# Performance work log

Measured on AMD Instinct MI355X. Metric: run time of the kernel, lower is better.

The kernel has to match this reference:

```python
import jax, jax.numpy as jnp
import numpy as np

N, K, D, E, H, O = 8192, 16, 256, 128, 512, 256


def _mlp(v, W1, W2):
    # nn.Sequential(Linear(no bias), Tanh, Linear(no bias)) with torch [out,in] weights
    return jnp.tanh(v @ W1.T) @ W2.T


def setup_inputs() -> dict:
    key = jax.random.key(0)
    ks = jax.random.split(key, 16)
    def rn(k, shape, s=1.0):
        return jax.random.normal(k, shape, jnp.float32) * s
    return {
        "x": rn(ks[0], (N, D)),
        "neibs": rn(ks[1], (N * K, D)),
        "edge_emb": rn(ks[2], (N * K, E)),
        "mask": jax.random.randint(ks[3], (N, K), 0, 2, jnp.int32),
        "W1x": rn(ks[4], (H, D), 0.02), "W2x": rn(ks[5], (H, H), 0.02),
        "W1n": rn(ks[6], (H, D), 0.02), "W2n": rn(ks[7], (H, H), 0.02),
        "W1e": rn(ks[8], (H, E), 0.02), "W2e": rn(ks[9], (H, H), 0.02),
        "Wfx": rn(ks[10], (O, D), 0.02), "bfx": jnp.zeros((O,), jnp.float32),
        "Wfn": rn(ks[11], (O, D), 0.02), "bfn": jnp.zeros((O,), jnp.float32),
        "Wfe": rn(ks[12], (O, E), 0.02), "bfe": jnp.zeros((O,), jnp.float32),
    }


def reference(x, neibs, edge_emb, mask, W1x, W2x, W1n, W2n, W1e, W2e,
              Wfx, bfx, Wfn, bfn, Wfe, bfe):
    n, d = x.shape
    e = edge_emb.shape[1]
    x_att = _mlp(x, W1x, W2x)                                  # [N,H]
    neib_att = _mlp(neibs, W1n, W2n).reshape(n, -1, H)         # [N,K,H]
    edge_att = _mlp(edge_emb, W1e, W2e).reshape(n, -1, H)      # [N,K,H]

    # node-neighbor attention (scaled by hard-coded sqrt(512))
    ws = jnp.einsum('nkh,nh->nk', neib_att, x_att) / np.sqrt(512.0).astype(np.float32)
    ws = jax.nn.softmax(ws, axis=1)
    agg_neib = jnp.einsum('nk,nkd->nd', ws, neibs.reshape(n, -1, d))
    out = jnp.concatenate([x @ Wfx.T + bfx, agg_neib @ Wfn.T + bfn], axis=1)

    # node-edge attention (unscaled, masked)
    ws2 = jnp.einsum('nkh,nh->nk', edge_att, x_att)
    ws2 = ws2 + (-9999999.0) * mask.astype(x.dtype)
    ws2 = jax.nn.softmax(ws2, axis=1)
    agg_edge = jnp.einsum('nk,nke->ne', ws2, edge_emb.reshape(n, -1, e))
    out = jnp.concatenate([out, agg_edge @ Wfe.T + bfe], axis=1)  # [N,3*O]
    return jax.nn.relu(out)
```

## Files before the change

### kernel.cpp

```cpp
#include <hip/hip_runtime.h>
#include <hip/hip_bf16.h>

typedef __bf16 bf16;
typedef __bf16 bf16x8 __attribute__((ext_vector_type(8)));
typedef float  f32x4  __attribute__((ext_vector_type(4)));

__device__ __forceinline__ void async16(const bf16* g, bf16* l) {
  __builtin_amdgcn_global_load_lds(
      (__attribute__((address_space(1))) void*)g,
      (__attribute__((address_space(3))) void*)l,
      16, 0, 0);
}

__device__ __forceinline__ void fence_barrier() {
  asm volatile("s_waitcnt vmcnt(0) lgkmcnt(0)" ::: "memory");
  __syncthreads();
}

__device__ __forceinline__ float fast_tanh(float x) {
  float e = __builtin_amdgcn_exp2f(x * 2.88539008177793f);
  return 1.f - 2.f * __builtin_amdgcn_rcpf(e + 1.f);
}

template<int ACT, typename OT>
__global__ __launch_bounds__(256, 4)
void gemm64(const bf16* __restrict__ A, const bf16* __restrict__ W,
            OT* __restrict__ C, int K, int ldc, float alpha,
            const float* __restrict__ bias) {
  __shared__ bf16 As[64 * 64];
  __shared__ bf16 Bs[64 * 64];
  const int tid  = threadIdx.x;
  const int wave = tid >> 6, lane = tid & 63;
  const int wr = wave >> 1, wc = wave & 1;
  const int g = lane >> 4, l4 = lane & 15;

  f32x4 acc[2][2];
#pragma unroll
  for (int i = 0; i < 2; ++i)
#pragma unroll
    for (int j = 0; j < 2; ++j)
      acc[i][j] = (f32x4){0.f, 0.f, 0.f, 0.f};

  const bf16* Abase = A + (size_t)blockIdx.x * 64 * K;
  const bf16* Wbase = W + (size_t)blockIdx.y * 64 * K;

  for (int k0 = 0; k0 < K; k0 += 64) {
#pragma unroll
    for (int i = 0; i < 2; ++i) {
      const int cb  = i * 256 + wave * 64;
      const int c   = cb + lane;
      const int row = c >> 3;
      const int kk  = (c & 7) << 3;
      async16(Abase + (size_t)row * K + k0 + kk, &As[cb * 8]);
      async16(Wbase + (size_t)row * K + k0 + kk, &Bs[cb * 8]);
    }
    fence_barrier();
#pragma unroll
    for (int s = 0; s < 2; ++s) {
      const int koff = s * 32 + g * 8;
      bf16x8 af[2], bfr[2];
#pragma unroll
      for (int i = 0; i < 2; ++i)
        af[i] = *(const bf16x8*)&As[(wr * 32 + i * 16 + l4) * 64 + koff];
#pragma unroll
      for (int j = 0; j < 2; ++j)
        bfr[j] = *(const bf16x8*)&Bs[(wc * 32 + j * 16 + l4) * 64 + koff];
#pragma unroll
      for (int i = 0; i < 2; ++i)
#pragma unroll
        for (int j = 0; j < 2; ++j)
          acc[i][j] = __builtin_amdgcn_mfma_f32_16x16x32_bf16(af[i], bfr[j], acc[i][j], 0, 0, 0);
    }
    fence_barrier();
  }

  const int rbase = blockIdx.x * 64 + wr * 32;
  const int cbase = blockIdx.y * 64 + wc * 32;
#pragma unroll
  for (int i = 0; i < 2; ++i)
#pragma unroll
    for (int j = 0; j < 2; ++j) {
      const int col = cbase + j * 16 + l4;
      const float bv = bias ? bias[col] : 0.f;
#pragma unroll
      for (int r = 0; r < 4; ++r) {
        const int row = rbase + i * 16 + g * 4 + r;
        float v = acc[i][j][r] * alpha + bv;
        if (ACT == 1) v = fast_tanh(v);
        if (ACT == 2) v = fmaxf(v, 0.f);
        C[(size_t)row * ldc + col] = (OT)v;
      }
    }
}

__global__ __launch_bounds__(256, 2)
void score_gemm(const bf16* __restrict__ A, const bf16* __restrict__ W,
                const bf16* __restrict__ y, int ldy, float* __restrict__ ws, int K) {
  __shared__ bf16 As[128 * 64];
  __shared__ bf16 Bs[128 * 64];
  const int tid  = threadIdx.x;
  const int wave = tid >> 6, lane = tid & 63;
  const int wr = wave >> 1, wc = wave & 1;
  const int g = lane >> 4, l4 = lane & 15;

  const bf16* Abase = A + (size_t)blockIdx.x * 128 * K;
  float p[4][4];
#pragma unroll
  for (int i = 0; i < 4; ++i)
#pragma unroll
    for (int r = 0; r < 4; ++r) p[i][r] = 0.f;

  const int rbase = blockIdx.x * 128 + wr * 64;

  for (int j = 0; j < 4; ++j) {
    const bf16* Wj = W + (size_t)j * 128 * K;
    f32x4 acc[4][4];
#pragma unroll
    for (int i = 0; i < 4; ++i)
#pragma unroll
      for (int jj = 0; jj < 4; ++jj)
        acc[i][jj] = (f32x4){0.f, 0.f, 0.f, 0.f};

    for (int k0 = 0; k0 < K; k0 += 64) {
#pragma unroll
      for (int i = 0; i < 4; ++i) {
        const int cb  = i * 256 + wave * 64;
        const int c   = cb + lane;
        const int row = c >> 3;
        const int kk  = (c & 7) << 3;
        async16(Abase + (size_t)row * K + k0 + kk, &As[cb * 8]);
        async16(Wj    + (size_t)row * K + k0 + kk, &Bs[cb * 8]);
      }
      fence_barrier();
#pragma unroll
      for (int s = 0; s < 2; ++s) {
        const int koff = s * 32 + g * 8;
        bf16x8 af[4], bfr[4];
#pragma unroll
        for (int i = 0; i < 4; ++i)
          af[i] = *(const bf16x8*)&As[(wr * 64 + i * 16 + l4) * 64 + koff];
#pragma unroll
        for (int jj = 0; jj < 4; ++jj)
          bfr[jj] = *(const bf16x8*)&Bs[(wc * 64 + jj * 16 + l4) * 64 + koff];
#pragma unroll
        for (int i = 0; i < 4; ++i)
#pragma unroll
          for (int jj = 0; jj < 4; ++jj)
            acc[i][jj] = __builtin_amdgcn_mfma_f32_16x16x32_bf16(af[i], bfr[jj], acc[i][jj], 0, 0, 0);
      }
      fence_barrier();
    }

#pragma unroll
    for (int i = 0; i < 4; ++i) {
      const int node = (rbase + i * 16) >> 4;
#pragma unroll
      for (int jj = 0; jj < 4; ++jj) {
        const float yv = (float)y[(size_t)node * ldy + j * 128 + wc * 64 + jj * 16 + l4];
        p[i][0] += fast_tanh(acc[i][jj][0]) * yv;
        p[i][1] += fast_tanh(acc[i][jj][1]) * yv;
        p[i][2] += fast_tanh(acc[i][jj][2]) * yv;
        p[i][3] += fast_tanh(acc[i][jj][3]) * yv;
      }
    }
  }

#pragma unroll
  for (int i = 0; i < 4; ++i)
#pragma unroll
    for (int r = 0; r < 4; ++r) {
      float v = p[i][r];
#pragma unroll
      for (int m = 1; m < 16; m <<= 1) v += __shfl_xor(v, m);
      p[i][r] = v;
    }
  if (l4 == 0) {
#pragma unroll
    for (int i = 0; i < 4; ++i)
#pragma unroll
      for (int r = 0; r < 4; ++r)
        atomicAdd(&ws[rbase + i * 16 + g * 4 + r], p[i][r]);
  }
}

__global__ void cvt_big(const float* __restrict__ s0, bf16* __restrict__ d0,
                        const float* __restrict__ s1, bf16* __restrict__ d1,
                        const float* __restrict__ s2, bf16* __restrict__ d2) {
  const int b = blockIdx.x;
  const float* s; bf16* d; size_t base;
  if (b < 1024)       { s = s0; d = d0; base = (size_t)b * 2048; }
  else if (b < 17408) { s = s1; d = d1; base = (size_t)(b - 1024) * 2048; }
  else                { s = s2; d = d2; base = (size_t)(b - 17408) * 2048; }
  const size_t i = base + (size_t)threadIdx.x * 8;
  const float4 a = *(const float4*)(s + i);
  const float4 c = *(const float4*)(s + i + 4);
  bf16x8 o = { (bf16)a.x, (bf16)a.y, (bf16)a.z, (bf16)a.w,
               (bf16)c.x, (bf16)c.y, (bf16)c.z, (bf16)c.w };
  *(bf16x8*)(d + i) = o;
}

struct CvtEnt { const float* s; bf16* d; int n; };
struct CvtArgs { CvtEnt e[7]; };

__global__ void cvt_small(CvtArgs args) {
  const CvtEnt ent = args.e[blockIdx.y];
  const int i = blockIdx.x * 2048 + threadIdx.x * 8;
  if (i < ent.n) {
    const float4 a = *(const float4*)(ent.s + i);
    const float4 c = *(const float4*)(ent.s + i + 4);
    bf16x8 o = { (bf16)a.x, (bf16)a.y, (bf16)a.z, (bf16)a.w,
                 (bf16)c.x, (bf16)c.y, (bf16)c.z, (bf16)c.w };
    *(bf16x8*)(ent.d + i) = o;
  }
}

__global__ void transpose512f(const float* __restrict__ s, bf16* __restrict__ d) {
  __shared__ float t[16][17];
  const int x0 = blockIdx.x * 16, y0 = blockIdx.y * 16;
  t[threadIdx.y][threadIdx.x] = s[(size_t)(y0 + threadIdx.y) * 512 + x0 + threadIdx.x];
  __syncthreads();
  d[(size_t)(x0 + threadIdx.y) * 512 + (y0 + threadIdx.x)] = (bf16)t[threadIdx.x][threadIdx.y];
}

__global__ void softmax_agg(const float* __restrict__ wsn, const float* __restrict__ wse,
                            const int* __restrict__ mask,
                            const bf16* __restrict__ neibs, const bf16* __restrict__ edge,
                            bf16* __restrict__ aggn, bf16* __restrict__ agge) {
  const int n = blockIdx.x;
  const int t = threadIdx.x;
  __shared__ float wn[16], we[16];
  if (t < 16) {
    wn[t] = wsn[n * 16 + t];
    we[t] = wse[n * 16 + t] - 9999999.0f * (float)mask[n * 16 + t];
  }
  __syncthreads();
  if (t == 0) {
    float m = wn[0];
    for (int k = 1; k < 16; ++k) m = fmaxf(m, wn[k]);
    float s = 0.f;
    for (int k = 0; k < 16; ++k) { wn[k] = expf(wn[k] - m); s += wn[k]; }
    s = 1.f / s;
    for (int k = 0; k < 16; ++k) wn[k] *= s;
  } else if (t == 64) {
    float m = we[0];
    for (int k = 1; k < 16; ++k) m = fmaxf(m, we[k]);
    float s = 0.f;
    for (int k = 0; k < 16; ++k) { we[k] = expf(we[k] - m); s += we[k]; }
    s = 1.f / s;
    for (int k = 0; k < 16; ++k) we[k] *= s;
  }
  __syncthreads();
  {
    const bf16* nb = neibs + (size_t)n * 16 * 256 + t;
    float a = 0.f;
#pragma unroll
    for (int k = 0; k < 16; ++k) a += wn[k] * (float)nb[(size_t)k * 256];
    aggn[(size_t)n * 256 + t] = (bf16)a;
  }
  if (t < 128) {
    const bf16* eb = edge + (size_t)n * 16 * 128 + t;
    float a = 0.f;
#pragma unroll
    for (int k = 0; k < 16; ++k) a += we[k] * (float)eb[(size_t)k * 128];
    agge[(size_t)n * 128 + t] = (bf16)a;
  }
}

extern "C" void kernel_launch(void* const* d_in, const int* in_sizes, int n_in,
                              void* d_out, int out_size, void* d_ws, size_t ws_size,
                              hipStream_t stream) {
  const float* x     = (const float*)d_in[0];
  const float* neibs = (const float*)d_in[1];
  const float* edge  = (const float*)d_in[2];
  const int*   mask  = (const int*)d_in[3];
  const float* W1x = (const float*)d_in[4];
  const float* W2x = (const float*)d_in[5];
  const float* W1n = (const float*)d_in[6];
  const float* W2n = (const float*)d_in[7];
  const float* W1e = (const float*)d_in[8];
  const float* W2e = (const float*)d_in[9];
  const float* Wfx = (const float*)d_in[10];
  const float* bfx = (const float*)d_in[11];
  const float* Wfn = (const float*)d_in[12];
  const float* bfn = (const float*)d_in[13];
  const float* Wfe = (const float*)d_in[14];
  const float* bfe = (const float*)d_in[15];
  float* out = (float*)d_out;

  char* wsb = (char*)d_ws;
  const size_t MB = 1024 * 1024;
  float* ws_n  = (float*)(wsb + 0);
  float* ws_e  = (float*)(wsb + 512 * 1024);
  bf16* W2nT   = (bf16*)(wsb + 1 * MB);
  bf16* W2eT   = (bf16*)(wsb + 1 * MB + 512 * 1024);
  bf16* h_x    = (bf16*)(wsb + 2 * MB);
  bf16* x_att  = (bf16*)(wsb + 10 * MB);
  bf16* agge   = (bf16*)(wsb + 14 * MB);
  bf16* y_n    = (bf16*)(wsb + 18 * MB);
  bf16* xb     = (bf16*)(wsb + 26 * MB);
  bf16* nb     = (bf16*)(wsb + 30 * MB);
  bf16* eb     = (bf16*)(wsb + 94 * MB);
  char* wtb    = wsb + 126 * MB;
  bf16* W1xb = (bf16*)(wtb + 0);
  bf16* W2xb = (bf16*)(wtb + 256 * 1024);
  bf16* W1nb = (bf16*)(wtb + 768 * 1024);
  bf16* W1eb = (bf16*)(wtb + 1024 * 1024);
  bf16* Wfxb = (bf16*)(wtb + 1152 * 1024);
  bf16* Wfnb = (bf16*)(wtb + 1280 * 1024);
  bf16* Wfeb = (bf16*)(wtb + 1408 * 1024);
  bf16* y_e  = h_x;
  bf16* aggn = x_att;

  const float inv_sqrt512 = 0.04419417382415922f;

  hipMemsetAsync(ws_n, 0, 1 * MB, stream);

  cvt_big<<<25600, 256, 0, stream>>>(x, xb, neibs, nb, edge, eb);

  CvtArgs ca;
  ca.e[0] = {W1x, W1xb, 131072};
  ca.e[1] = {W2x, W2xb, 262144};
  ca.e[2] = {W1n, W1nb, 131072};
  ca.e[3] = {W1e, W1eb, 65536};
  ca.e[4] = {Wfx, Wfxb, 65536};
  ca.e[5] = {Wfn, Wfnb, 65536};
  ca.e[6] = {Wfe, Wfeb, 32768};
  cvt_small<<<dim3(128, 7), 256, 0, stream>>>(ca);

  transpose512f<<<dim3(32, 32), dim3(16, 16), 0, stream>>>(W2n, W2nT);
  transpose512f<<<dim3(32, 32), dim3(16, 16), 0, stream>>>(W2e, W2eT);

  gemm64<1, bf16><<<dim3(128, 8), 256, 0, stream>>>(xb, W1xb, h_x, 256, 512, 1.f, nullptr);
  gemm64<0, bf16><<<dim3(128, 8), 256, 0, stream>>>(h_x, W2xb, x_att, 512, 512, 1.f, nullptr);
  gemm64<0, bf16><<<dim3(128, 8), 256, 0, stream>>>(x_att, W2nT, y_n, 512, 512, inv_sqrt512, nullptr);
  gemm64<0, bf16><<<dim3(128, 8), 256, 0, stream>>>(x_att, W2eT, y_e, 512, 512, 1.f, nullptr);

  score_gemm<<<1024, 256, 0, stream>>>(nb, W1nb, y_n, 512, ws_n, 256);
  score_gemm<<<1024, 256, 0, stream>>>(eb, W1eb, y_e, 512, ws_e, 128);

  softmax_agg<<<8192, 256, 0, stream>>>(ws_n, ws_e, mask, nb, eb, aggn, agge);

  gemm64<2, float><<<dim3(128, 4), 256, 0, stream>>>(xb,   Wfxb, out + 0,   256, 768, 1.f, bfx);
  gemm64<2, float><<<dim3(128, 4), 256, 0, stream>>>(aggn, Wfnb, out + 256, 256, 768, 1.f, bfn);
  gemm64<2, float><<<dim3(128, 4), 256, 0, stream>>>(agge, Wfeb, out + 512, 128, 768, 1.f, bfe);
}
```

Measured before the change: 480.7 us.

## Fuse fp32 load, score GEMM, softmax and aggregation into one kernel

Neighbor and edge embeddings are now read as fp32 and converted to bf16 in LDS inside a new score_agg kernel. That kernel computes the attention scores, masks, takes the softmax and does the weighted aggregation from the same LDS tile. This removes the large bf16 copies of neibs and edge, the atomics plus memset for scores, and the separate softmax_agg pass that re-read the embeddings. The two y projections become one wider GEMM over contiguous W2nT/W2eT, with the 1/sqrt(512) scale moved into the score step. The two transposes also merge into one launch. The trade-off is a block that holds a whole 64-row A tile in LDS, which could limit occupancy.

```diff
diff --git a/kernel.cpp b/kernel.cpp
--- a/kernel.cpp
+++ b/kernel.cpp
@@ -2,6 +2,8 @@
 #include <hip/hip_bf16.h>
 
 typedef __bf16 bf16;
+typedef __bf16 bf16x2 __attribute__((ext_vector_type(2)));
+typedef __bf16 bf16x4 __attribute__((ext_vector_type(4)));
 typedef __bf16 bf16x8 __attribute__((ext_vector_type(8)));
 typedef float  f32x4  __attribute__((ext_vector_type(4)));
 
@@ -93,27 +95,42 @@
     }
 }
 
+template<int D>
 __global__ __launch_bounds__(256, 2)
-void score_gemm(const bf16* __restrict__ A, const bf16* __restrict__ W,
-                const bf16* __restrict__ y, int ldy, float* __restrict__ ws, int K) {
-  __shared__ bf16 As[128 * 64];
-  __shared__ bf16 Bs[128 * 64];
+void score_agg(const float* __restrict__ A, const bf16* __restrict__ Wb,
+               const bf16* __restrict__ y, int ldy, int yoff, float scale,
+               const int* __restrict__ mask, bf16* __restrict__ agg) {
+  __shared__ bf16 As[64 * D];
+  __shared__ bf16 Bs[256 * 64];
+  float* sred = (float*)Bs;
+  float* wgt  = (float*)Bs + 256;
   const int tid  = threadIdx.x;
   const int wave = tid >> 6, lane = tid & 63;
-  const int wr = wave >> 1, wc = wave & 1;
   const int g = lane >> 4, l4 = lane & 15;
-
-  const bf16* Abase = A + (size_t)blockIdx.x * 128 * K;
+  const int blk = blockIdx.x;
+
+  const float* Ab = A + (size_t)blk * 64 * D;
+  constexpr int F4PR = D / 4;
+#pragma unroll
+  for (int ii = 0; ii < D / 16; ++ii) {
+    const int c    = ii * 256 + tid;
+    const int row  = c / F4PR;
+    const int col4 = (c % F4PR) * 4;
+    const float4 v = *(const float4*)(Ab + (size_t)row * D + col4);
+    bf16x4 o = {(bf16)v.x, (bf16)v.y, (bf16)v.z, (bf16)v.w};
+    *(bf16x4*)&As[row * D + col4] = o;
+  }
+
   float p[4][4];
 #pragma unroll
   for (int i = 0; i < 4; ++i)
 #pragma unroll
     for (int r = 0; r < 4; ++r) p[i][r] = 0.f;
 
-  const int rbase = blockIdx.x * 128 + wr * 64;
-
-  for (int j = 0; j < 4; ++j) {
-    const bf16* Wj = W + (size_t)j * 128 * K;
+  fence_barrier();
+
+  for (int j = 0; j < 2; ++j) {
+    const bf16* Wj = Wb + (size_t)j * 256 * D;
     f32x4 acc[4][4];
 #pragma unroll
     for (int i = 0; i < 4; ++i)
@@ -121,15 +138,14 @@
       for (int jj = 0; jj < 4; ++jj)
         acc[i][jj] = (f32x4){0.f, 0.f, 0.f, 0.f};
 
-    for (int k0 = 0; k0 < K; k0 += 64) {
-#pragma unroll
-      for (int i = 0; i < 4; ++i) {
+    for (int k0 = 0; k0 < D; k0 += 64) {
+#pragma unroll
+      for (int i = 0; i < 8; ++i) {
         const int cb  = i * 256 + wave * 64;
         const int c   = cb + lane;
         const int row = c >> 3;
         const int kk  = (c & 7) << 3;
-        async16(Abase + (size_t)row * K + k0 + kk, &As[cb * 8]);
-        async16(Wj    + (size_t)row * K + k0 + kk, &Bs[cb * 8]);
+        async16(Wj + (size_t)row * D + k0 + kk, &Bs[cb * 8]);
       }
       fence_barrier();
 #pragma unroll
@@ -138,10 +154,10 @@
         bf16x8 af[4], bfr[4];
 #pragma unroll
         for (int i = 0; i < 4; ++i)
-          af[i] = *(const bf16x8*)&As[(wr * 64 + i * 16 + l4) * 64 + koff];
+          af[i] = *(const bf16x8*)&As[(i * 16 + l4) * D + k0 + koff];
 #pragma unroll
         for (int jj = 0; jj < 4; ++jj)
-          bfr[jj] = *(const bf16x8*)&Bs[(wc * 64 + jj * 16 + l4) * 64 + koff];
+          bfr[jj] = *(const bf16x8*)&Bs[(wave * 64 + jj * 16 + l4) * 64 + koff];
 #pragma unroll
         for (int i = 0; i < 4; ++i)
 #pragma unroll
@@ -153,10 +169,10 @@
 
 #pragma unroll
     for (int i = 0; i < 4; ++i) {
-      const int node = (rbase + i * 16) >> 4;
+      const size_t yb = (size_t)(blk * 4 + i) * ldy + yoff + j * 256 + wave * 64;
 #pragma unroll
       for (int jj = 0; jj < 4; ++jj) {
-        const float yv = (float)y[(size_t)node * ldy + j * 128 + wc * 64 + jj * 16 + l4];
+        const float yv = (float)y[yb + jj * 16 + l4];
         p[i][0] += fast_tanh(acc[i][jj][0]) * yv;
         p[i][1] += fast_tanh(acc[i][jj][1]) * yv;
         p[i][2] += fast_tanh(acc[i][jj][2]) * yv;
@@ -179,28 +195,54 @@
     for (int i = 0; i < 4; ++i)
 #pragma unroll
       for (int r = 0; r < 4; ++r)
-        atomicAdd(&ws[rbase + i * 16 + g * 4 + r], p[i][r]);
-  }
-}
-
-__global__ void cvt_big(const float* __restrict__ s0, bf16* __restrict__ d0,
-                        const float* __restrict__ s1, bf16* __restrict__ d1,
-                        const float* __restrict__ s2, bf16* __restrict__ d2) {
-  const int b = blockIdx.x;
-  const float* s; bf16* d; size_t base;
-  if (b < 1024)       { s = s0; d = d0; base = (size_t)b * 2048; }
-  else if (b < 17408) { s = s1; d = d1; base = (size_t)(b - 1024) * 2048; }
-  else                { s = s2; d = d2; base = (size_t)(b - 17408) * 2048; }
-  const size_t i = base + (size_t)threadIdx.x * 8;
-  const float4 a = *(const float4*)(s + i);
-  const float4 c = *(const float4*)(s + i + 4);
-  bf16x8 o = { (bf16)a.x, (bf16)a.y, (bf16)a.z, (bf16)a.w,
-               (bf16)c.x, (bf16)c.y, (bf16)c.z, (bf16)c.w };
-  *(bf16x8*)(d + i) = o;
+        sred[wave * 64 + i * 16 + g * 4 + r] = p[i][r];
+  }
+  __syncthreads();
+
+  if (tid < 64) {
+    const int node_g = blk * 4 + (tid >> 4);
+    float s = (sred[tid] + sred[64 + tid] + sred[128 + tid] + sred[192 + tid]) * scale;
+    if (mask) s -= 9999999.0f * (float)mask[node_g * 16 + (tid & 15)];
+    float m = s;
+#pragma unroll
+    for (int d = 1; d < 16; d <<= 1) m = fmaxf(m, __shfl_xor(m, d));
+    float e = __builtin_amdgcn_exp2f((s - m) * 1.44269504088896f);
+    float sum = e;
+#pragma unroll
+    for (int d = 1; d < 16; d <<= 1) sum += __shfl_xor(sum, d);
+    wgt[tid] = e / sum;
+  }
+  __syncthreads();
+
+  constexpr int EPT = D / 64;
+  const int n  = tid >> 6;
+  const int dl = (tid & 63) * EPT;
+  float a[EPT];
+#pragma unroll
+  for (int e = 0; e < EPT; ++e) a[e] = 0.f;
+#pragma unroll
+  for (int k = 0; k < 16; ++k) {
+    const float w = wgt[n * 16 + k];
+    if constexpr (EPT == 4) {
+      bf16x4 v = *(const bf16x4*)&As[(n * 16 + k) * D + dl];
+      a[0] += w * (float)v[0]; a[1] += w * (float)v[1];
+      a[2] += w * (float)v[2]; a[3] += w * (float)v[3];
+    } else {
+      bf16x2 v = *(const bf16x2*)&As[(n * 16 + k) * D + dl];
+      a[0] += w * (float)v[0]; a[1] += w * (float)v[1];
+    }
+  }
+  if constexpr (EPT == 4) {
+    bf16x4 o = {(bf16)a[0], (bf16)a[1], (bf16)a[2], (bf16)a[3]};
+    *(bf16x4*)&agg[(size_t)(blk * 4 + n) * D + dl] = o;
+  } else {
+    bf16x2 o = {(bf16)a[0], (bf16)a[1]};
+    *(bf16x2*)&agg[(size_t)(blk * 4 + n) * D + dl] = o;
+  }
 }
 
 struct CvtEnt { const float* s; bf16* d; int n; };
-struct CvtArgs { CvtEnt e[7]; };
+struct CvtArgs { CvtEnt e[8]; };
 
 __global__ void cvt_small(CvtArgs args) {
   const CvtEnt ent = args.e[blockIdx.y];
@@ -214,56 +256,15 @@
   }
 }
 
-__global__ void transpose512f(const float* __restrict__ s, bf16* __restrict__ d) {
+__global__ void transpose2(const float* __restrict__ s0, bf16* __restrict__ d0,
+                           const float* __restrict__ s1, bf16* __restrict__ d1) {
   __shared__ float t[16][17];
+  const float* s = blockIdx.z ? s1 : s0;
+  bf16* d = blockIdx.z ? d1 : d0;
   const int x0 = blockIdx.x * 16, y0 = blockIdx.y * 16;
   t[threadIdx.y][threadIdx.x] = s[(size_t)(y0 + threadIdx.y) * 512 + x0 + threadIdx.x];
   __syncthreads();
   d[(size_t)(x0 + threadIdx.y) * 512 + (y0 + threadIdx.x)] = (bf16)t[threadIdx.x][threadIdx.y];
-}
-
-__global__ void softmax_agg(const float* __restrict__ wsn, const float* __restrict__ wse,
-                            const int* __restrict__ mask,
-                            const bf16* __restrict__ neibs, const bf16* __restrict__ edge,
-                            bf16* __restrict__ aggn, bf16* __restrict__ agge) {
-  const int n = blockIdx.x;
-  const int t = threadIdx.x;
-  __shared__ float wn[16], we[16];
-  if (t < 16) {
-    wn[t] = wsn[n * 16 + t];
-    we[t] = wse[n * 16 + t] - 9999999.0f * (float)mask[n * 16 + t];
-  }
-  __syncthreads();
-  if (t == 0) {
-    float m = wn[0];
-    for (int k = 1; k < 16; ++k) m = fmaxf(m, wn[k]);
-    float s = 0.f;
-    for (int k = 0; k < 16; ++k) { wn[k] = expf(wn[k] - m); s += wn[k]; }
-    s = 1.f / s;
-    for (int k = 0; k < 16; ++k) wn[k] *= s;
-  } else if (t == 64) {
-    float m = we[0];
-    for (int k = 1; k < 16; ++k) m = fmaxf(m, we[k]);
-    float s = 0.f;
-    for (int k = 0; k < 16; ++k) { we[k] = expf(we[k] - m); s += we[k]; }
-    s = 1.f / s;
-    for (int k = 0; k < 16; ++k) we[k] *= s;
-  }
-  __syncthreads();
-  {
-    const bf16* nb = neibs + (size_t)n * 16 * 256 + t;
-    float a = 0.f;
-#pragma unroll
-    for (int k = 0; k < 16; ++k) a += wn[k] * (float)nb[(size_t)k * 256];
-    aggn[(size_t)n * 256 + t] = (bf16)a;
-  }
-  if (t < 128) {
-    const bf16* eb = edge + (size_t)n * 16 * 128 + t;
-    float a = 0.f;
-#pragma unroll
-    for (int k = 0; k < 16; ++k) a += we[k] * (float)eb[(size_t)k * 128];
-    agge[(size_t)n * 128 + t] = (bf16)a;
-  }
 }
 
 extern "C" void kernel_launch(void* const* d_in, const int* in_sizes, int n_in,
@@ -289,18 +290,9 @@
 
   char* wsb = (char*)d_ws;
   const size_t MB = 1024 * 1024;
-  float* ws_n  = (float*)(wsb + 0);
-  float* ws_e  = (float*)(wsb + 512 * 1024);
-  bf16* W2nT   = (bf16*)(wsb + 1 * MB);
-  bf16* W2eT   = (bf16*)(wsb + 1 * MB + 512 * 1024);
-  bf16* h_x    = (bf16*)(wsb + 2 * MB);
-  bf16* x_att  = (bf16*)(wsb + 10 * MB);
-  bf16* agge   = (bf16*)(wsb + 14 * MB);
-  bf16* y_n    = (bf16*)(wsb + 18 * MB);
-  bf16* xb     = (bf16*)(wsb + 26 * MB);
-  bf16* nb     = (bf16*)(wsb + 30 * MB);
-  bf16* eb     = (bf16*)(wsb + 94 * MB);
-  char* wtb    = wsb + 126 * MB;
+  bf16* W2nT = (bf16*)(wsb + 0);
+  bf16* W2eT = (bf16*)(wsb + 512 * 1024);
+  char* wtb  = wsb + 1 * MB;
   bf16* W1xb = (bf16*)(wtb + 0);
   bf16* W2xb = (bf16*)(wtb + 256 * 1024);
   bf16* W1nb = (bf16*)(wtb + 768 * 1024);
@@ -308,37 +300,34 @@
   bf16* Wfxb = (bf16*)(wtb + 1152 * 1024);
   bf16* Wfnb = (bf16*)(wtb + 1280 * 1024);
   bf16* Wfeb = (bf16*)(wtb + 1408 * 1024);
-  bf16* y_e  = h_x;
-  bf16* aggn = x_att;
+  bf16* xb    = (bf16*)(wsb + 3 * MB);
+  bf16* h_x   = (bf16*)(wsb + 7 * MB);
+  bf16* x_att = (bf16*)(wsb + 15 * MB);
+  bf16* ycat  = (bf16*)(wsb + 23 * MB);
+  bf16* aggn  = (bf16*)(wsb + 39 * MB);
+  bf16* agge  = (bf16*)(wsb + 43 * MB);
 
   const float inv_sqrt512 = 0.04419417382415922f;
 
-  hipMemsetAsync(ws_n, 0, 1 * MB, stream);
-
-  cvt_big<<<25600, 256, 0, stream>>>(x, xb, neibs, nb, edge, eb);
-
   CvtArgs ca;
-  ca.e[0] = {W1x, W1xb, 131072};
-  ca.e[1] = {W2x, W2xb, 262144};
-  ca.e[2] = {W1n, W1nb, 131072};
-  ca.e[3] = {W1e, W1eb, 65536};
-  ca.e[4] = {Wfx, Wfxb, 65536};
-  ca.e[5] = {Wfn, Wfnb, 65536};
-  ca.e[6] = {Wfe, Wfeb, 32768};
-  cvt_small<<<dim3(128, 7), 256, 0, stream>>>(ca);
-
-  transpose512f<<<dim3(32, 32), dim3(16, 16), 0, stream>>>(W2n, W2nT);
-  transpose512f<<<dim3(32, 32), dim3(16, 16), 0, stream>>>(W2e, W2eT);
+  ca.e[0] = {x,   xb,   2097152};
+  ca.e[1] = {W1x, W1xb, 131072};
+  ca.e[2] = {W2x, W2xb, 262144};
+  ca.e[3] = {W1n, W1nb, 131072};
+  ca.e[4] = {W1e, W1eb, 65536};
+  ca.e[5] = {Wfx, Wfxb, 65536};
+  ca.e[6] = {Wfn, Wfnb, 65536};
+  ca.e[7] = {Wfe, Wfeb, 32768};
+  cvt_small<<<dim3(1024, 8), 256, 0, stream>>>(ca);
+
+  transpose2<<<dim3(32, 32, 2), dim3(16, 16), 0, stream>>>(W2n, W2nT, W2e, W2eT);
 
   gemm64<1, bf16><<<dim3(128, 8), 256, 0, stream>>>(xb, W1xb, h_x, 256, 512, 1.f, nullptr);
   gemm64<0, bf16><<<dim3(128, 8), 256, 0, stream>>>(h_x, W2xb, x_att, 512, 512, 1.f, nullptr);
-  gemm64<0, bf16><<<dim3(128, 8), 256, 0, stream>>>(x_att, W2nT, y_n, 512, 512, inv_sqrt512, nullptr);
-  gemm64<0, bf16><<<dim3(128, 8), 256, 0, stream>>>(x_att, W2eT, y_e, 512, 512, 1.f, nullptr);
-
-  score_gemm<<<1024, 256, 0, stream>>>(nb, W1nb, y_n, 512, ws_n, 256);
-  score_gemm<<<1024, 256, 0, stream>>>(eb, W1eb, y_e, 512, ws_e, 128);
-
-  softmax_agg<<<8192, 256, 0, stream>>>(ws_n, ws_e, mask, nb, eb, aggn, agge);
+  gemm64<0, bf16><<<dim3(128, 16), 256, 0, stream>>>(x_att, W2nT, ycat, 512, 1024, 1.f, nullptr);
+
+  score_agg<256><<<2048, 256, 0, stream>>>(neibs, W1nb, ycat, 1024, 0, inv_sqrt512, nullptr, aggn);
+  score_agg<128><<<2048, 256, 0, stream>>>(edge,  W1eb, ycat, 1024, 512, 1.f, mask, agge);
 
   gemm64<2, float><<<dim3(128, 4), 256, 0, stream>>>(xb,   Wfxb, out + 0,   256, 768, 1.f, bfx);
   gemm64<2, float><<<dim3(128, 4), 256, 0, stream>>>(aggn, Wfnb, out + 256, 256, 768, 1.f, bfn);
```

Result: faster. 428.8 us (-10.8%).
